# Performance work log

Hardware: AMD Instinct MI355X
Metric: run time of the kernel (lower is better)

Reference implementation:

```python
import jax, jax.numpy as jnp
import numpy as np

B, N, C1, C2, H = 4, 4096, 320, 256, 5
HD = C1 // H  # 64


def setup_inputs() -> dict:
    key = jax.random.key(0)
    ks = jax.random.split(key, 9)
    w = lambda k, shape, fan_in: jax.random.normal(k, shape, jnp.float32) * (fan_in ** -0.5)
    return {
        "x1": jax.random.normal(ks[0], (B, N, C1), jnp.float32),
        "x2": jax.random.normal(ks[1], (B, N, C2), jnp.float32),
        # nn.Linear weights, torch layout [out_features, in_features]
        "q1_w": w(ks[2], (C1, C1), C1),
        "q2_w": w(ks[3], (C1, C2), C2),
        "kv1_w": w(ks[4], (2 * C1, C2), C2),
        "kv2_w": w(ks[5], (2 * C1, C1), C1),
        "proj1_w": w(ks[6], (C1, C1), C1),
        "proj1_b": jnp.zeros((C1,), jnp.float32),
        "proj2_w": w(ks[7], (C1, C1), C1),
        "proj2_b": jnp.zeros((C1,), jnp.float32),
    }


def _branch(xq, xkv, q_w, kv_w, proj_w, proj_b):
    b, n, _ = xq.shape
    scale = HD ** -0.5
    q = (xq @ q_w.T).reshape(b, n, H, HD).transpose(0, 2, 1, 3)          # [B,H,N,HD]
    kv = (xkv @ kv_w.T).reshape(b, n, 2, H, HD).transpose(2, 0, 3, 1, 4)  # [2,B,H,N,HD]
    k, v = kv[0], kv[1]
    attn = jax.nn.softmax(jnp.einsum('bhqd,bhkd->bhqk', q * scale, k), axis=-1)
    y = jnp.einsum('bhqk,bhkd->bhqd', attn, v)                            # [B,H,N,HD]
    y = y.transpose(0, 2, 1, 3).reshape(b, n, C1)
    return y @ proj_w.T + proj_b


def reference(x1, x2, q1_w, q2_w, kv1_w, kv2_w, proj1_w, proj1_b, proj2_w, proj2_b):
    y1 = _branch(x1, x2, q1_w, kv1_w, proj1_w, proj1_b)  # x1 queries, x2 keys/values
    y2 = _branch(x2, x1, q2_w, kv2_w, proj2_w, proj2_b)  # x2 queries, x1 keys/values
    return jnp.concatenate((y1, y2), axis=-1)            # [B,N,2*C1]
```

## Files before the change

### kernel.cpp

```cpp
#include <hip/hip_runtime.h>
#include <hip/hip_bf16.h>

#define Bb 4
#define Nn 4096
#define C1 320
#define C2 256
#define Hh 5
#define HD 64
#define Mm (Bb*Nn)

using bf16 = __hip_bfloat16;
typedef __attribute__((ext_vector_type(8))) short  short8;
typedef __attribute__((ext_vector_type(4))) short  short4_;
typedef __attribute__((ext_vector_type(4))) float  f32x4;
typedef __attribute__((ext_vector_type(16))) float f32x16;

__device__ __forceinline__ short f2s(float f) {
    bf16 h = __float2bfloat16(f);
    short s;
    __builtin_memcpy(&s, &h, 2);
    return s;
}

__device__ __forceinline__ float fexp2(float x) {
#if __has_builtin(__builtin_amdgcn_exp2f)
    return __builtin_amdgcn_exp2f(x);
#else
    return exp2f(x);
#endif
}

__device__ __forceinline__ int swz(int row, int bb) {
    return row * 64 + ((bb ^ (row & 7)) << 3);
}

__device__ __forceinline__ unsigned cvtpk(float lo, float hi) {
    unsigned r;
    asm("v_cvt_pk_bf16_f32 %0, %1, %2" : "=v"(r) : "v"(lo), "v"(hi));
    return r;
}

__device__ __forceinline__ void plswap(unsigned &a, unsigned &b) {
#if __has_builtin(__builtin_amdgcn_permlane32_swap)
    auto r = __builtin_amdgcn_permlane32_swap(a, b, false, false);
    a = r[0]; b = r[1];
#else
    asm("v_permlane32_swap_b32 %0, %1" : "+v"(a), "+v"(b));
#endif
}

__device__ __forceinline__ short8 mk8(unsigned d0, unsigned d1, unsigned d2, unsigned d3) {
    union { unsigned u[4]; short8 s; } u;
    u.u[0] = d0; u.u[1] = d1; u.u[2] = d2; u.u[3] = d3;
    return u.s;
}

struct CvtArgs {
    const float* s[8];
    bf16* d[8];
    int off[9];
};

__global__ void cvt_all(CvtArgs a) {
    int i = (blockIdx.x * blockDim.x + threadIdx.x) * 4;
    if (i >= a.off[8]) return;
    int seg = 0;
    #pragma unroll
    for (int k = 1; k < 8; ++k) seg += (i >= a.off[k]);
    int j = i - a.off[seg];
    float4 v = *(const float4*)(a.s[seg] + j);
    short4_ o = { f2s(v.x), f2s(v.y), f2s(v.z), f2s(v.w) };
    *(short4_*)(a.d[seg] + j) = o;
}

__global__ __launch_bounds__(256) void gemm_bt(
    const bf16* __restrict__ A, const bf16* __restrict__ W,
    int K, int mode, float oscale,
    bf16* __restrict__ O1, bf16* __restrict__ O2,
    const float* __restrict__ bias, float* __restrict__ Of, int ooff)
{
    __shared__ bf16 la[64 * 64];
    __shared__ bf16 lw[64 * 64];
    const int m0 = blockIdx.x * 64, n0 = blockIdx.y * 64;
    const int t = threadIdx.x;
    const int wave = t >> 6, lane = t & 63, l16 = lane & 15, quad = lane >> 4;
    const int sr = t >> 3, sb = t & 7;

    f32x4 acc[4] = {{0.f,0.f,0.f,0.f},{0.f,0.f,0.f,0.f},{0.f,0.f,0.f,0.f},{0.f,0.f,0.f,0.f}};

    const int nk = K >> 6;
    short8 ra0 = *(const short8*)(A + (size_t)(m0 + sr) * K + sb * 8);
    short8 ra1 = *(const short8*)(A + (size_t)(m0 + sr + 32) * K + sb * 8);
    short8 rw0 = *(const short8*)(W + (size_t)(n0 + sr) * K + sb * 8);
    short8 rw1 = *(const short8*)(W + (size_t)(n0 + sr + 32) * K + sb * 8);

    for (int kt = 0; kt < nk; ++kt) {
        __syncthreads();
        *(short8*)&la[swz(sr, sb)]      = ra0;
        *(short8*)&la[swz(sr + 32, sb)] = ra1;
        *(short8*)&lw[swz(sr, sb)]      = rw0;
        *(short8*)&lw[swz(sr + 32, sb)] = rw1;
        __syncthreads();
        if (kt + 1 < nk) {
            const int k0 = (kt + 1) * 64;
            ra0 = *(const short8*)(A + (size_t)(m0 + sr) * K + k0 + sb * 8);
            ra1 = *(const short8*)(A + (size_t)(m0 + sr + 32) * K + k0 + sb * 8);
            rw0 = *(const short8*)(W + (size_t)(n0 + sr) * K + k0 + sb * 8);
            rw1 = *(const short8*)(W + (size_t)(n0 + sr + 32) * K + k0 + sb * 8);
        }
        const int arow = wave * 16 + l16;
        short8 a0 = *(const short8*)&la[swz(arow, quad)];
        short8 a1 = *(const short8*)&la[swz(arow, quad + 4)];
        #pragma unroll
        for (int nt = 0; nt < 4; ++nt) {
            const int brow = nt * 16 + l16;
            short8 b0 = *(const short8*)&lw[swz(brow, quad)];
            short8 b1 = *(const short8*)&lw[swz(brow, quad + 4)];
            acc[nt] = __builtin_amdgcn_mfma_f32_16x16x32_bf16(a0, b0, acc[nt], 0, 0, 0);
            acc[nt] = __builtin_amdgcn_mfma_f32_16x16x32_bf16(a1, b1, acc[nt], 0, 0, 0);
        }
    }

    const int mrow = m0 + wave * 16 + quad * 4;
    if (mode == 2) {
        #pragma unroll
        for (int nt = 0; nt < 4; ++nt) {
            int col = n0 + nt * 16 + l16;
            float bv = bias[col];
            #pragma unroll
            for (int r = 0; r < 4; ++r)
                Of[(size_t)(mrow + r) * 640 + ooff + col] = acc[nt][r] + bv;
        }
    } else if (mode == 0 || n0 < C1) {
        #pragma unroll
        for (int nt = 0; nt < 4; ++nt) {
            int col = n0 + nt * 16 + l16;
            #pragma unroll
            for (int r = 0; r < 4; ++r)
                O1[(size_t)(mrow + r) * C1 + col] = __float2bfloat16(acc[nt][r] * oscale);
        }
    } else {
        #pragma unroll
        for (int nt = 0; nt < 4; ++nt) {
            int col = n0 + nt * 16 + l16 - C1;
            int h = col >> 6, d = col & 63;
            #pragma unroll
            for (int r = 0; r < 4; ++r) {
                int m = mrow + r;
                int b = m >> 12, n = m & (Nn - 1);
                O2[((size_t)(b * Hh + h) * 64 + d) * Nn + n] = __float2bfloat16(acc[nt][r]);
            }
        }
    }
}

__global__ __launch_bounds__(256, 2) void flash_kernel(
    const bf16* __restrict__ Q1, const bf16* __restrict__ K1,
    const bf16* __restrict__ V1, bf16* __restrict__ Y1,
    const bf16* __restrict__ Q2, const bf16* __restrict__ K2,
    const bf16* __restrict__ V2, bf16* __restrict__ Y2)
{
    __shared__ bf16 lk[64 * 64];
    __shared__ bf16 lv[64 * 64];
    const int qt = blockIdx.x, h = blockIdx.y, z = blockIdx.z;
    const int b = z & 3, branch = z >> 2;
    const bf16* Q  = branch ? Q2 : Q1;
    const bf16* Km = branch ? K2 : K1;
    const bf16* Vt = branch ? V2 : V1;
    bf16*       Yo = branch ? Y2 : Y1;

    const int t = threadIdx.x;
    const int wave = t >> 6, lane = t & 63;
    const int l32 = lane & 31, hi = lane >> 5;
    const int sr = t >> 3, sb = t & 7;

    const int qrow0 = qt * 256 + wave * 64;

    short8 qf[2][4];
    #pragma unroll
    for (int qb = 0; qb < 2; ++qb) {
        const bf16* qptr = Q + (size_t)(b * Nn + qrow0 + qb * 32 + l32) * C1 + h * HD + hi * 8;
        #pragma unroll
        for (int ksd = 0; ksd < 4; ++ksd)
            qf[qb][ksd] = *(const short8*)(qptr + ksd * 16);
    }

    f32x16 o[2][2];
    #pragma unroll
    for (int qb = 0; qb < 2; ++qb)
        #pragma unroll
        for (int db = 0; db < 2; ++db)
            o[qb][db] = (f32x16){0.f,0.f,0.f,0.f,0.f,0.f,0.f,0.f,0.f,0.f,0.f,0.f,0.f,0.f,0.f,0.f};
    float lsum[2] = {0.f, 0.f};

    const bf16* Kbase = Km + (size_t)b * Nn * C1 + h * HD;
    const bf16* Vbase = Vt + (size_t)(b * Hh + h) * 64 * Nn;

    short8 rk0 = *(const short8*)(Kbase + (size_t)sr * C1 + sb * 8);
    short8 rk1 = *(const short8*)(Kbase + (size_t)(sr + 32) * C1 + sb * 8);
    short8 rv0 = *(const short8*)(Vbase + (size_t)sr * Nn + sb * 8);
    short8 rv1 = *(const short8*)(Vbase + (size_t)(sr + 32) * Nn + sb * 8);

    const int NT = Nn / 64;
    for (int kt = 0; kt < NT; ++kt) {
        __syncthreads();
        *(short8*)&lk[swz(sr, sb)]      = rk0;
        *(short8*)&lk[swz(sr + 32, sb)] = rk1;
        *(short8*)&lv[swz(sr, sb)]      = rv0;
        *(short8*)&lv[swz(sr + 32, sb)] = rv1;
        __syncthreads();
        if (kt + 1 < NT) {
            const int kn = (kt + 1) * 64;
            rk0 = *(const short8*)(Kbase + (size_t)(kn + sr) * C1 + sb * 8);
            rk1 = *(const short8*)(Kbase + (size_t)(kn + sr + 32) * C1 + sb * 8);
            rv0 = *(const short8*)(Vbase + (size_t)sr * Nn + kn + sb * 8);
            rv1 = *(const short8*)(Vbase + (size_t)(sr + 32) * Nn + kn + sb * 8);
        }

        #pragma unroll
        for (int kb = 0; kb < 2; ++kb) {
            short8 ka[4];
            #pragma unroll
            for (int ksd = 0; ksd < 4; ++ksd)
                ka[ksd] = *(const short8*)&lk[swz(kb * 32 + l32, ksd * 2 + hi)];

            short8 pa[2][2];
            #pragma unroll
            for (int qb = 0; qb < 2; ++qb) {
                f32x16 s = (f32x16){0.f,0.f,0.f,0.f,0.f,0.f,0.f,0.f,0.f,0.f,0.f,0.f,0.f,0.f,0.f,0.f};
                #pragma unroll
                for (int ksd = 0; ksd < 4; ++ksd)
                    s = __builtin_amdgcn_mfma_f32_32x32x16_bf16(ka[ksd], qf[qb][ksd], s, 0, 0, 0);
                float p[16];
                #pragma unroll
                for (int r = 0; r < 16; ++r) p[r] = fexp2(s[r]);
                lsum[qb] += (((p[0]+p[1])+(p[2]+p[3])) + ((p[4]+p[5])+(p[6]+p[7])))
                          + (((p[8]+p[9])+(p[10]+p[11])) + ((p[12]+p[13])+(p[14]+p[15])));
                unsigned d0 = cvtpk(p[0],  p[1]),  d2 = cvtpk(p[4],  p[5]);
                plswap(d0, d2);
                unsigned d1 = cvtpk(p[2],  p[3]),  d3 = cvtpk(p[6],  p[7]);
                plswap(d1, d3);
                pa[qb][0] = mk8(d0, d1, d2, d3);
                unsigned e0 = cvtpk(p[8],  p[9]),  e2 = cvtpk(p[12], p[13]);
                plswap(e0, e2);
                unsigned e1 = cvtpk(p[10], p[11]), e3 = cvtpk(p[14], p[15]);
                plswap(e1, e3);
                pa[qb][1] = mk8(e0, e1, e2, e3);
            }

            #pragma unroll
            for (int ks = 0; ks < 2; ++ks) {
                #pragma unroll
                for (int db = 0; db < 2; ++db) {
                    short8 bv = *(const short8*)&lv[swz(db * 32 + l32, kb * 4 + ks * 2 + hi)];
                    o[0][db] = __builtin_amdgcn_mfma_f32_32x32x16_bf16(pa[0][ks], bv, o[0][db], 0, 0, 0);
                    o[1][db] = __builtin_amdgcn_mfma_f32_32x32x16_bf16(pa[1][ks], bv, o[1][db], 0, 0, 0);
                }
            }
        }
    }

    #pragma unroll
    for (int qb = 0; qb < 2; ++qb) {
        float l = lsum[qb] + __shfl_xor(lsum[qb], 32, 64);
        float inv = 1.0f / l;
        #pragma unroll
        for (int r = 0; r < 16; ++r) {
            const int qr = (r & 3) + 8 * (r >> 2) + 4 * hi;
            float invr = __shfl(inv, qr, 64);
            size_t row = (size_t)(b * Nn + qrow0 + qb * 32 + qr);
            #pragma unroll
            for (int db = 0; db < 2; ++db)
                Yo[row * C1 + h * HD + db * 32 + l32] = __float2bfloat16(o[qb][db][r] * invr);
        }
    }
}

extern "C" void kernel_launch(void* const* d_in, const int* in_sizes, int n_in,
                              void* d_out, int out_size, void* d_ws, size_t ws_size,
                              hipStream_t stream)
{
    const float* x1   = (const float*)d_in[0];
    const float* x2   = (const float*)d_in[1];
    const float* q1w  = (const float*)d_in[2];
    const float* q2w  = (const float*)d_in[3];
    const float* kv1w = (const float*)d_in[4];
    const float* kv2w = (const float*)d_in[5];
    const float* p1w  = (const float*)d_in[6];
    const float* p1b  = (const float*)d_in[7];
    const float* p2w  = (const float*)d_in[8];
    const float* p2b  = (const float*)d_in[9];
    float* out = (float*)d_out;

    bf16* ws = (bf16*)d_ws;
    size_t o = 0;
    bf16* x1b  = ws + o; o += (size_t)Mm * C1;
    bf16* x2b  = ws + o; o += (size_t)Mm * C2;
    bf16* wq1  = ws + o; o += C1 * C1;
    bf16* wq2  = ws + o; o += C1 * C2;
    bf16* wkv1 = ws + o; o += 2 * C1 * C2;
    bf16* wkv2 = ws + o; o += 2 * C1 * C1;
    bf16* wp1  = ws + o; o += C1 * C1;
    bf16* wp2  = ws + o; o += C1 * C1;
    bf16* Q1   = ws + o; o += (size_t)Mm * C1;
    bf16* K1   = ws + o; o += (size_t)Mm * C1;
    bf16* V1t  = ws + o; o += (size_t)Mm * C1;
    bf16* Q2   = ws + o; o += (size_t)Mm * C1;
    bf16* K2   = ws + o; o += (size_t)Mm * C1;
    bf16* V2t  = ws + o; o += (size_t)Mm * C1;
    bf16* Y1   = ws + o; o += (size_t)Mm * C1;
    bf16* Y2   = ws + o; o += (size_t)Mm * C1;
    (void)ws_size; (void)in_sizes; (void)n_in; (void)out_size;

    CvtArgs ca;
    ca.s[0] = x1;   ca.d[0] = x1b;  int n0 = Mm * C1;
    ca.s[1] = x2;   ca.d[1] = x2b;  int n1 = Mm * C2;
    ca.s[2] = q1w;  ca.d[2] = wq1;  int n2 = C1 * C1;
    ca.s[3] = q2w;  ca.d[3] = wq2;  int n3 = C1 * C2;
    ca.s[4] = kv1w; ca.d[4] = wkv1; int n4 = 2 * C1 * C2;
    ca.s[5] = kv2w; ca.d[5] = wkv2; int n5 = 2 * C1 * C1;
    ca.s[6] = p1w;  ca.d[6] = wp1;  int n6 = C1 * C1;
    ca.s[7] = p2w;  ca.d[7] = wp2;  int n7 = C1 * C1;
    int ns[8] = {n0, n1, n2, n3, n4, n5, n6, n7};
    ca.off[0] = 0;
    for (int i = 0; i < 8; ++i) ca.off[i + 1] = ca.off[i] + ns[i];
    int total = ca.off[8];
    cvt_all<<<dim3((total / 4 + 255) / 256), 256, 0, stream>>>(ca);

    const float QS = 0.125f * 1.4426950408889634f;

    gemm_bt<<<dim3(Mm / 64, C1 / 64), 256, 0, stream>>>(x1b, wq1, C1, 0, QS, Q1, nullptr, nullptr, nullptr, 0);
    gemm_bt<<<dim3(Mm / 64, (2 * C1) / 64), 256, 0, stream>>>(x2b, wkv1, C2, 1, 1.0f, K1, V1t, nullptr, nullptr, 0);
    gemm_bt<<<dim3(Mm / 64, C1 / 64), 256, 0, stream>>>(x2b, wq2, C2, 0, QS, Q2, nullptr, nullptr, nullptr, 0);
    gemm_bt<<<dim3(Mm / 64, (2 * C1) / 64), 256, 0, stream>>>(x1b, wkv2, C1, 1, 1.0f, K2, V2t, nullptr, nullptr, 0);

    flash_kernel<<<dim3(Nn / 256, Hh, 2 * Bb), 256, 0, stream>>>(Q1, K1, V1t, Y1, Q2, K2, V2t, Y2);

    gemm_bt<<<dim3(Mm / 64, C1 / 64), 256, 0, stream>>>(Y1, wp1, C1, 2, 1.0f, nullptr, nullptr, p1b, out, 0);
    gemm_bt<<<dim3(Mm / 64, C1 / 64), 256, 0, stream>>>(Y2, wp2, C1, 2, 1.0f, nullptr, nullptr, p2b, out, C1);
}
```

Measured before the change: 351.6 us.

## Double-buffer K/V tiles in LDS, compute row sums via MFMA, add setprio

The flash kernel now keeps two LDS buffers for K and V. The next tile is written into the other buffer while the current one is being computed, which cuts the loop to one barrier per iteration and lets loads run two tiles ahead. The softmax denominator now comes from extra MFMAs against a ones vector instead of scalar adds and cross-lane shuffles. It also uses bf16-rounded probabilities, which slightly changes numerics. s_setprio hints are placed around the MFMA groups. The cost is double the LDS use, which may affect occupancy at 2 blocks/CU, plus four more MFMAs per kb step.

```diff
diff --git a/kernel.cpp b/kernel.cpp
--- a/kernel.cpp
+++ b/kernel.cpp
@@ -160,8 +160,8 @@
     const bf16* __restrict__ Q2, const bf16* __restrict__ K2,
     const bf16* __restrict__ V2, bf16* __restrict__ Y2)
 {
-    __shared__ bf16 lk[64 * 64];
-    __shared__ bf16 lv[64 * 64];
+    __shared__ bf16 lk[2][64 * 64];
+    __shared__ bf16 lv[2][64 * 64];
     const int qt = blockIdx.x, h = blockIdx.y, z = blockIdx.z;
     const int b = z & 3, branch = z >> 2;
     const bf16* Q  = branch ? Q2 : Q1;
@@ -185,36 +185,63 @@
             qf[qb][ksd] = *(const short8*)(qptr + ksd * 16);
     }
 
+    const f32x16 Z = {0.f,0.f,0.f,0.f,0.f,0.f,0.f,0.f,0.f,0.f,0.f,0.f,0.f,0.f,0.f,0.f};
+    const short  one_bf = (short)0x3F80;
+    const short8 ONESB = {one_bf,one_bf,one_bf,one_bf,one_bf,one_bf,one_bf,one_bf};
+
     f32x16 o[2][2];
+    f32x16 lacc[2];
     #pragma unroll
-    for (int qb = 0; qb < 2; ++qb)
-        #pragma unroll
-        for (int db = 0; db < 2; ++db)
-            o[qb][db] = (f32x16){0.f,0.f,0.f,0.f,0.f,0.f,0.f,0.f,0.f,0.f,0.f,0.f,0.f,0.f,0.f,0.f};
-    float lsum[2] = {0.f, 0.f};
+    for (int qb = 0; qb < 2; ++qb) {
+        lacc[qb] = Z;
+        #pragma unroll
+        for (int db = 0; db < 2; ++db) o[qb][db] = Z;
+    }
 
     const bf16* Kbase = Km + (size_t)b * Nn * C1 + h * HD;
     const bf16* Vbase = Vt + (size_t)(b * Hh + h) * 64 * Nn;
 
-    short8 rk0 = *(const short8*)(Kbase + (size_t)sr * C1 + sb * 8);
-    short8 rk1 = *(const short8*)(Kbase + (size_t)(sr + 32) * C1 + sb * 8);
-    short8 rv0 = *(const short8*)(Vbase + (size_t)sr * Nn + sb * 8);
-    short8 rv1 = *(const short8*)(Vbase + (size_t)(sr + 32) * Nn + sb * 8);
+    const bf16* kp0 = Kbase + (size_t)sr * C1 + sb * 8;
+    const bf16* kp1 = kp0 + (size_t)32 * C1;
+    const bf16* vp0 = Vbase + (size_t)sr * Nn + sb * 8;
+    const bf16* vp1 = vp0 + (size_t)32 * Nn;
+
+    short8 rk0 = *(const short8*)kp0;
+    short8 rk1 = *(const short8*)kp1;
+    short8 rv0 = *(const short8*)vp0;
+    short8 rv1 = *(const short8*)vp1;
+    kp0 += 64 * C1; kp1 += 64 * C1; vp0 += 64; vp1 += 64;
+    *(short8*)&lk[0][swz(sr, sb)]      = rk0;
+    *(short8*)&lk[0][swz(sr + 32, sb)] = rk1;
+    *(short8*)&lv[0][swz(sr, sb)]      = rv0;
+    *(short8*)&lv[0][swz(sr + 32, sb)] = rv1;
+    rk0 = *(const short8*)kp0;
+    rk1 = *(const short8*)kp1;
+    rv0 = *(const short8*)vp0;
+    rv1 = *(const short8*)vp1;
+    kp0 += 64 * C1; kp1 += 64 * C1; vp0 += 64; vp1 += 64;
+    __syncthreads();
 
     const int NT = Nn / 64;
     for (int kt = 0; kt < NT; ++kt) {
-        __syncthreads();
-        *(short8*)&lk[swz(sr, sb)]      = rk0;
-        *(short8*)&lk[swz(sr + 32, sb)] = rk1;
-        *(short8*)&lv[swz(sr, sb)]      = rv0;
-        *(short8*)&lv[swz(sr + 32, sb)] = rv1;
-        __syncthreads();
+        const int cur = kt & 1;
+        const bf16* LK = lk[cur];
+        const bf16* LV = lv[cur];
+
         if (kt + 1 < NT) {
-            const int kn = (kt + 1) * 64;
-            rk0 = *(const short8*)(Kbase + (size_t)(kn + sr) * C1 + sb * 8);
-            rk1 = *(const short8*)(Kbase + (size_t)(kn + sr + 32) * C1 + sb * 8);
-            rv0 = *(const short8*)(Vbase + (size_t)sr * Nn + kn + sb * 8);
-            rv1 = *(const short8*)(Vbase + (size_t)(sr + 32) * Nn + kn + sb * 8);
+            bf16* WK = lk[cur ^ 1];
+            bf16* WV = lv[cur ^ 1];
+            *(short8*)&WK[swz(sr, sb)]      = rk0;
+            *(short8*)&WK[swz(sr + 32, sb)] = rk1;
+            *(short8*)&WV[swz(sr, sb)]      = rv0;
+            *(short8*)&WV[swz(sr + 32, sb)] = rv1;
+        }
+        if (kt + 2 < NT) {
+            rk0 = *(const short8*)kp0;
+            rk1 = *(const short8*)kp1;
+            rv0 = *(const short8*)vp0;
+            rv1 = *(const short8*)vp1;
+            kp0 += 64 * C1; kp1 += 64 * C1; vp0 += 64; vp1 += 64;
         }
 
         #pragma unroll
@@ -222,20 +249,20 @@
             short8 ka[4];
             #pragma unroll
             for (int ksd = 0; ksd < 4; ++ksd)
-                ka[ksd] = *(const short8*)&lk[swz(kb * 32 + l32, ksd * 2 + hi)];
+                ka[ksd] = *(const short8*)&LK[swz(kb * 32 + l32, ksd * 2 + hi)];
 
             short8 pa[2][2];
             #pragma unroll
             for (int qb = 0; qb < 2; ++qb) {
-                f32x16 s = (f32x16){0.f,0.f,0.f,0.f,0.f,0.f,0.f,0.f,0.f,0.f,0.f,0.f,0.f,0.f,0.f,0.f};
-                #pragma unroll
-                for (int ksd = 0; ksd < 4; ++ksd)
-                    s = __builtin_amdgcn_mfma_f32_32x32x16_bf16(ka[ksd], qf[qb][ksd], s, 0, 0, 0);
+                __builtin_amdgcn_s_setprio(1);
+                f32x16 s = __builtin_amdgcn_mfma_f32_32x32x16_bf16(ka[0], qf[qb][0], Z, 0, 0, 0);
+                s = __builtin_amdgcn_mfma_f32_32x32x16_bf16(ka[1], qf[qb][1], s, 0, 0, 0);
+                s = __builtin_amdgcn_mfma_f32_32x32x16_bf16(ka[2], qf[qb][2], s, 0, 0, 0);
+                s = __builtin_amdgcn_mfma_f32_32x32x16_bf16(ka[3], qf[qb][3], s, 0, 0, 0);
+                __builtin_amdgcn_s_setprio(0);
                 float p[16];
                 #pragma unroll
                 for (int r = 0; r < 16; ++r) p[r] = fexp2(s[r]);
-                lsum[qb] += (((p[0]+p[1])+(p[2]+p[3])) + ((p[4]+p[5])+(p[6]+p[7])))
-                          + (((p[8]+p[9])+(p[10]+p[11])) + ((p[12]+p[13])+(p[14]+p[15])));
                 unsigned d0 = cvtpk(p[0],  p[1]),  d2 = cvtpk(p[4],  p[5]);
                 plswap(d0, d2);
                 unsigned d1 = cvtpk(p[2],  p[3]),  d3 = cvtpk(p[6],  p[7]);
@@ -248,26 +275,29 @@
                 pa[qb][1] = mk8(e0, e1, e2, e3);
             }
 
+            __builtin_amdgcn_s_setprio(1);
             #pragma unroll
             for (int ks = 0; ks < 2; ++ks) {
                 #pragma unroll
                 for (int db = 0; db < 2; ++db) {
-                    short8 bv = *(const short8*)&lv[swz(db * 32 + l32, kb * 4 + ks * 2 + hi)];
+                    short8 bv = *(const short8*)&LV[swz(db * 32 + l32, kb * 4 + ks * 2 + hi)];
                     o[0][db] = __builtin_amdgcn_mfma_f32_32x32x16_bf16(pa[0][ks], bv, o[0][db], 0, 0, 0);
                     o[1][db] = __builtin_amdgcn_mfma_f32_32x32x16_bf16(pa[1][ks], bv, o[1][db], 0, 0, 0);
                 }
+                lacc[0] = __builtin_amdgcn_mfma_f32_32x32x16_bf16(pa[0][ks], ONESB, lacc[0], 0, 0, 0);
+                lacc[1] = __builtin_amdgcn_mfma_f32_32x32x16_bf16(pa[1][ks], ONESB, lacc[1], 0, 0, 0);
             }
-        }
+            __builtin_amdgcn_s_setprio(0);
+        }
+        __syncthreads();
     }
 
     #pragma unroll
     for (int qb = 0; qb < 2; ++qb) {
-        float l = lsum[qb] + __shfl_xor(lsum[qb], 32, 64);
-        float inv = 1.0f / l;
         #pragma unroll
         for (int r = 0; r < 16; ++r) {
             const int qr = (r & 3) + 8 * (r >> 2) + 4 * hi;
-            float invr = __shfl(inv, qr, 64);
+            float invr = 1.0f / lacc[qb][r];
             size_t row = (size_t)(b * Nn + qrow0 + qb * 32 + qr);
             #pragma unroll
             for (int db = 0; db < 2; ++db)
```

Result: slower. 366.5 us (+4.2%).

## Split flash attention key range across two wave groups with LDS reduction

Applied to the files above, without the earlier changes.

Doubles the flash kernel block to 512 threads, with waves 0-3 and waves 4-7 each processing half of the key sequence (0-2047 vs 2048-4095) for the same 256 query rows. Each group loads its own 32-key tile per iteration, and at the end the partial row sums and output accumulators are combined through shared memory before the first group normalizes and writes. This is meant to raise the number of waves in flight and cover latency, since the grid only has 640 blocks. In exchange it adds a final reduction with several barriers and more register pressure under the new 512,4 launch bound.

```diff
diff --git a/kernel.cpp b/kernel.cpp
--- a/kernel.cpp
+++ b/kernel.cpp
@@ -154,7 +154,7 @@
     }
 }
 
-__global__ __launch_bounds__(256, 2) void flash_kernel(
+__global__ __launch_bounds__(512, 4) void flash_kernel(
     const bf16* __restrict__ Q1, const bf16* __restrict__ K1,
     const bf16* __restrict__ V1, bf16* __restrict__ Y1,
     const bf16* __restrict__ Q2, const bf16* __restrict__ K2,
@@ -172,9 +172,10 @@
     const int t = threadIdx.x;
     const int wave = t >> 6, lane = t & 63;
     const int l32 = lane & 31, hi = lane >> 5;
+    const int qw = wave & 3, khalf = wave >> 2;
     const int sr = t >> 3, sb = t & 7;
 
-    const int qrow0 = qt * 256 + wave * 64;
+    const int qrow0 = qt * 256 + qw * 64;
 
     short8 qf[2][4];
     #pragma unroll
@@ -196,82 +197,109 @@
     const bf16* Kbase = Km + (size_t)b * Nn * C1 + h * HD;
     const bf16* Vbase = Vt + (size_t)(b * Hh + h) * 64 * Nn;
 
-    short8 rk0 = *(const short8*)(Kbase + (size_t)sr * C1 + sb * 8);
-    short8 rk1 = *(const short8*)(Kbase + (size_t)(sr + 32) * C1 + sb * 8);
-    short8 rv0 = *(const short8*)(Vbase + (size_t)sr * Nn + sb * 8);
-    short8 rv1 = *(const short8*)(Vbase + (size_t)(sr + 32) * Nn + sb * 8);
-
-    const int NT = Nn / 64;
+    const bf16* kp = Kbase + (size_t)((sr >> 5) * 2048 + (sr & 31)) * C1 + sb * 8;
+    const bf16* vp = Vbase + (size_t)sr * Nn + (sb >> 2) * 2048 + (sb & 3) * 8;
+    short8 rk = *(const short8*)kp;
+    short8 rv = *(const short8*)vp;
+
+    const int NT = 2048 / 32;
     for (int kt = 0; kt < NT; ++kt) {
         __syncthreads();
-        *(short8*)&lk[swz(sr, sb)]      = rk0;
-        *(short8*)&lk[swz(sr + 32, sb)] = rk1;
-        *(short8*)&lv[swz(sr, sb)]      = rv0;
-        *(short8*)&lv[swz(sr + 32, sb)] = rv1;
+        *(short8*)&lk[swz(sr, sb)] = rk;
+        *(short8*)&lv[swz(sr, sb)] = rv;
         __syncthreads();
         if (kt + 1 < NT) {
-            const int kn = (kt + 1) * 64;
-            rk0 = *(const short8*)(Kbase + (size_t)(kn + sr) * C1 + sb * 8);
-            rk1 = *(const short8*)(Kbase + (size_t)(kn + sr + 32) * C1 + sb * 8);
-            rv0 = *(const short8*)(Vbase + (size_t)sr * Nn + kn + sb * 8);
-            rv1 = *(const short8*)(Vbase + (size_t)(sr + 32) * Nn + kn + sb * 8);
-        }
-
-        #pragma unroll
-        for (int kb = 0; kb < 2; ++kb) {
-            short8 ka[4];
+            kp += 32 * C1; vp += 32;
+            rk = *(const short8*)kp;
+            rv = *(const short8*)vp;
+        }
+
+        short8 ka[4];
+        #pragma unroll
+        for (int ksd = 0; ksd < 4; ++ksd)
+            ka[ksd] = *(const short8*)&lk[swz(khalf * 32 + l32, ksd * 2 + hi)];
+
+        short8 pa[2][2];
+        #pragma unroll
+        for (int qb = 0; qb < 2; ++qb) {
+            f32x16 s = (f32x16){0.f,0.f,0.f,0.f,0.f,0.f,0.f,0.f,0.f,0.f,0.f,0.f,0.f,0.f,0.f,0.f};
             #pragma unroll
             for (int ksd = 0; ksd < 4; ++ksd)
-                ka[ksd] = *(const short8*)&lk[swz(kb * 32 + l32, ksd * 2 + hi)];
-
-            short8 pa[2][2];
-            #pragma unroll
-            for (int qb = 0; qb < 2; ++qb) {
-                f32x16 s = (f32x16){0.f,0.f,0.f,0.f,0.f,0.f,0.f,0.f,0.f,0.f,0.f,0.f,0.f,0.f,0.f,0.f};
-                #pragma unroll
-                for (int ksd = 0; ksd < 4; ++ksd)
-                    s = __builtin_amdgcn_mfma_f32_32x32x16_bf16(ka[ksd], qf[qb][ksd], s, 0, 0, 0);
-                float p[16];
-                #pragma unroll
-                for (int r = 0; r < 16; ++r) p[r] = fexp2(s[r]);
-                lsum[qb] += (((p[0]+p[1])+(p[2]+p[3])) + ((p[4]+p[5])+(p[6]+p[7])))
-                          + (((p[8]+p[9])+(p[10]+p[11])) + ((p[12]+p[13])+(p[14]+p[15])));
-                unsigned d0 = cvtpk(p[0],  p[1]),  d2 = cvtpk(p[4],  p[5]);
-                plswap(d0, d2);
-                unsigned d1 = cvtpk(p[2],  p[3]),  d3 = cvtpk(p[6],  p[7]);
-                plswap(d1, d3);
-                pa[qb][0] = mk8(d0, d1, d2, d3);
-                unsigned e0 = cvtpk(p[8],  p[9]),  e2 = cvtpk(p[12], p[13]);
-                plswap(e0, e2);
-                unsigned e1 = cvtpk(p[10], p[11]), e3 = cvtpk(p[14], p[15]);
-                plswap(e1, e3);
-                pa[qb][1] = mk8(e0, e1, e2, e3);
-            }
-
-            #pragma unroll
-            for (int ks = 0; ks < 2; ++ks) {
-                #pragma unroll
-                for (int db = 0; db < 2; ++db) {
-                    short8 bv = *(const short8*)&lv[swz(db * 32 + l32, kb * 4 + ks * 2 + hi)];
-                    o[0][db] = __builtin_amdgcn_mfma_f32_32x32x16_bf16(pa[0][ks], bv, o[0][db], 0, 0, 0);
-                    o[1][db] = __builtin_amdgcn_mfma_f32_32x32x16_bf16(pa[1][ks], bv, o[1][db], 0, 0, 0);
-                }
-            }
-        }
-    }
+                s = __builtin_amdgcn_mfma_f32_32x32x16_bf16(ka[ksd], qf[qb][ksd], s, 0, 0, 0);
+            float p[16];
+            #pragma unroll
+            for (int r = 0; r < 16; ++r) p[r] = fexp2(s[r]);
+            lsum[qb] += (((p[0]+p[1])+(p[2]+p[3])) + ((p[4]+p[5])+(p[6]+p[7])))
+                      + (((p[8]+p[9])+(p[10]+p[11])) + ((p[12]+p[13])+(p[14]+p[15])));
+            unsigned d0 = cvtpk(p[0],  p[1]),  d2 = cvtpk(p[4],  p[5]);
+            plswap(d0, d2);
+            unsigned d1 = cvtpk(p[2],  p[3]),  d3 = cvtpk(p[6],  p[7]);
+            plswap(d1, d3);
+            pa[qb][0] = mk8(d0, d1, d2, d3);
+            unsigned e0 = cvtpk(p[8],  p[9]),  e2 = cvtpk(p[12], p[13]);
+            plswap(e0, e2);
+            unsigned e1 = cvtpk(p[10], p[11]), e3 = cvtpk(p[14], p[15]);
+            plswap(e1, e3);
+            pa[qb][1] = mk8(e0, e1, e2, e3);
+        }
+
+        #pragma unroll
+        for (int ks = 0; ks < 2; ++ks) {
+            #pragma unroll
+            for (int db = 0; db < 2; ++db) {
+                short8 bv = *(const short8*)&lv[swz(db * 32 + l32, khalf * 4 + ks * 2 + hi)];
+                o[0][db] = __builtin_amdgcn_mfma_f32_32x32x16_bf16(pa[0][ks], bv, o[0][db], 0, 0, 0);
+                o[1][db] = __builtin_amdgcn_mfma_f32_32x32x16_bf16(pa[1][ks], bv, o[1][db], 0, 0, 0);
+            }
+        }
+    }
+
+    __syncthreads();
+    float* sk = (float*)lk;
+    float* sv = (float*)lv;
+    const int idx = qw * 64 + lane;
+
+    if (khalf == 1) { sk[idx] = lsum[0]; sk[256 + idx] = lsum[1]; }
+    __syncthreads();
+    if (khalf == 0) { lsum[0] += sk[idx]; lsum[1] += sk[256 + idx]; }
 
     #pragma unroll
     for (int qb = 0; qb < 2; ++qb) {
-        float l = lsum[qb] + __shfl_xor(lsum[qb], 32, 64);
-        float inv = 1.0f / l;
-        #pragma unroll
-        for (int r = 0; r < 16; ++r) {
-            const int qr = (r & 3) + 8 * (r >> 2) + 4 * hi;
-            float invr = __shfl(inv, qr, 64);
-            size_t row = (size_t)(b * Nn + qrow0 + qb * 32 + qr);
-            #pragma unroll
-            for (int db = 0; db < 2; ++db)
-                Yo[row * C1 + h * HD + db * 32 + l32] = __float2bfloat16(o[qb][db][r] * invr);
+        #pragma unroll
+        for (int db = 0; db < 2; ++db) {
+            __syncthreads();
+            if (khalf == 1) {
+                #pragma unroll
+                for (int r = 0; r < 16; ++r) {
+                    float* dst = (r < 8) ? sk : sv;
+                    dst[(r & 7) * 256 + idx] = o[qb][db][r];
+                }
+            }
+            __syncthreads();
+            if (khalf == 0) {
+                #pragma unroll
+                for (int r = 0; r < 16; ++r) {
+                    const float* src = (r < 8) ? sk : sv;
+                    o[qb][db][r] += src[(r & 7) * 256 + idx];
+                }
+            }
+        }
+    }
+
+    if (khalf == 0) {
+        #pragma unroll
+        for (int qb = 0; qb < 2; ++qb) {
+            float l = lsum[qb] + __shfl_xor(lsum[qb], 32, 64);
+            float inv = 1.0f / l;
+            #pragma unroll
+            for (int r = 0; r < 16; ++r) {
+                const int qr = (r & 3) + 8 * (r >> 2) + 4 * hi;
+                float invr = __shfl(inv, qr, 64);
+                size_t row = (size_t)(b * Nn + qrow0 + qb * 32 + qr);
+                #pragma unroll
+                for (int db = 0; db < 2; ++db)
+                    Yo[row * C1 + h * HD + db * 32 + l32] = __float2bfloat16(o[qb][db][r] * invr);
+            }
         }
     }
 }
@@ -334,7 +362,7 @@
     gemm_bt<<<dim3(Mm / 64, C1 / 64), 256, 0, stream>>>(x2b, wq2, C2, 0, QS, Q2, nullptr, nullptr, nullptr, 0);
     gemm_bt<<<dim3(Mm / 64, (2 * C1) / 64), 256, 0, stream>>>(x1b, wkv2, C1, 1, 1.0f, K2, V2t, nullptr, nullptr, 0);
 
-    flash_kernel<<<dim3(Nn / 256, Hh, 2 * Bb), 256, 0, stream>>>(Q1, K1, V1t, Y1, Q2, K2, V2t, Y2);
+    flash_kernel<<<dim3(Nn / 256, Hh, 2 * Bb), 512, 0, stream>>>(Q1, K1, V1t, Y1, Q2, K2, V2t, Y2);
 
     gemm_bt<<<dim3(Mm / 64, C1 / 64), 256, 0, stream>>>(Y1, wp1, C1, 2, 1.0f, nullptr, nullptr, p1b, out, 0);
     gemm_bt<<<dim3(Mm / 64, C1 / 64), 256, 0, stream>>>(Y2, wp2, C1, 2, 1.0f, nullptr, nullptr, p2b, out, C1);
```

New measurement: 796.9 us. 127% more time.

## Merge projection GEMMs per input and enlarge GEMM tiles to 128 rows

Applied to the files above, without the earlier changes.

The four Q/KV projection GEMMs become two launches, one per input activation. Each launch computes both the Q and the KV outputs for that input, so the input is shared across one grid. The two output-projection GEMMs become a single launch with a z dimension. The M tile grows from 64 to 128 rows, so each wave computes two 16-row fragments and reuses the B fragments from shared memory. This cuts launch count and the number of times weights are reloaded, at the cost of more registers and LDS per block and fewer blocks.

```diff
diff --git a/kernel.cpp b/kernel.cpp
--- a/kernel.cpp
+++ b/kernel.cpp
@@ -13,7 +13,6 @@
 typedef __attribute__((ext_vector_type(8))) short  short8;
 typedef __attribute__((ext_vector_type(4))) short  short4_;
 typedef __attribute__((ext_vector_type(4))) float  f32x4;
-typedef __attribute__((ext_vector_type(16))) float f32x16;
 
 __device__ __forceinline__ short f2s(float f) {
     bf16 h = __float2bfloat16(f);
@@ -32,6 +31,209 @@
 
 __device__ __forceinline__ int swz(int row, int bb) {
     return row * 64 + ((bb ^ (row & 7)) << 3);
+}
+
+struct CvtArgs {
+    const float* s[8];
+    bf16* d[8];
+    int off[9];
+};
+
+__global__ void cvt_all(CvtArgs a) {
+    int i = (blockIdx.x * blockDim.x + threadIdx.x) * 4;
+    if (i >= a.off[8]) return;
+    int seg = 0;
+    #pragma unroll
+    for (int k = 1; k < 8; ++k) seg += (i >= a.off[k]);
+    int j = i - a.off[seg];
+    float4 v = *(const float4*)(a.s[seg] + j);
+    short4_ o = { f2s(v.x), f2s(v.y), f2s(v.z), f2s(v.w) };
+    *(short4_*)(a.d[seg] + j) = o;
+}
+
+__global__ __launch_bounds__(256) void gemm_proj(
+    const bf16* __restrict__ A, const bf16* __restrict__ Wq,
+    const bf16* __restrict__ Wkv, int K, float qs,
+    bf16* __restrict__ Qo, bf16* __restrict__ Ko, bf16* __restrict__ Vo)
+{
+    __shared__ bf16 la[128 * 64];
+    __shared__ bf16 lw[64 * 64];
+    const int m0 = blockIdx.x * 128;
+    const bool isq = blockIdx.y < 5;
+    const bf16* W = isq ? Wq : Wkv;
+    const int n0 = (isq ? blockIdx.y : blockIdx.y - 5) * 64;
+    const int t = threadIdx.x;
+    const int wave = t >> 6, lane = t & 63, l16 = lane & 15, quad = lane >> 4;
+    const int sr = t >> 3, sb = t & 7;
+
+    f32x4 acc[2][4];
+    #pragma unroll
+    for (int mf = 0; mf < 2; ++mf)
+        #pragma unroll
+        for (int nt = 0; nt < 4; ++nt) acc[mf][nt] = {0.f,0.f,0.f,0.f};
+
+    const int nk = K >> 6;
+    const bf16* ap = A + (size_t)(m0 + sr) * K + sb * 8;
+    const bf16* wp = W + (size_t)(n0 + sr) * K + sb * 8;
+    short8 ra0 = *(const short8*)ap;
+    short8 ra1 = *(const short8*)(ap + (size_t)32 * K);
+    short8 ra2 = *(const short8*)(ap + (size_t)64 * K);
+    short8 ra3 = *(const short8*)(ap + (size_t)96 * K);
+    short8 rw0 = *(const short8*)wp;
+    short8 rw1 = *(const short8*)(wp + (size_t)32 * K);
+
+    for (int kt = 0; kt < nk; ++kt) {
+        __syncthreads();
+        *(short8*)&la[swz(sr,      sb)] = ra0;
+        *(short8*)&la[swz(sr + 32, sb)] = ra1;
+        *(short8*)&la[swz(sr + 64, sb)] = ra2;
+        *(short8*)&la[swz(sr + 96, sb)] = ra3;
+        *(short8*)&lw[swz(sr,      sb)] = rw0;
+        *(short8*)&lw[swz(sr + 32, sb)] = rw1;
+        __syncthreads();
+        if (kt + 1 < nk) {
+            ap += 64; wp += 64;
+            ra0 = *(const short8*)ap;
+            ra1 = *(const short8*)(ap + (size_t)32 * K);
+            ra2 = *(const short8*)(ap + (size_t)64 * K);
+            ra3 = *(const short8*)(ap + (size_t)96 * K);
+            rw0 = *(const short8*)wp;
+            rw1 = *(const short8*)(wp + (size_t)32 * K);
+        }
+        const int arow = wave * 32 + l16;
+        short8 a00 = *(const short8*)&la[swz(arow,      quad)];
+        short8 a01 = *(const short8*)&la[swz(arow,      quad + 4)];
+        short8 a10 = *(const short8*)&la[swz(arow + 16, quad)];
+        short8 a11 = *(const short8*)&la[swz(arow + 16, quad + 4)];
+        #pragma unroll
+        for (int nt = 0; nt < 4; ++nt) {
+            const int brow = nt * 16 + l16;
+            short8 b0 = *(const short8*)&lw[swz(brow, quad)];
+            short8 b1 = *(const short8*)&lw[swz(brow, quad + 4)];
+            acc[0][nt] = __builtin_amdgcn_mfma_f32_16x16x32_bf16(a00, b0, acc[0][nt], 0, 0, 0);
+            acc[0][nt] = __builtin_amdgcn_mfma_f32_16x16x32_bf16(a01, b1, acc[0][nt], 0, 0, 0);
+            acc[1][nt] = __builtin_amdgcn_mfma_f32_16x16x32_bf16(a10, b0, acc[1][nt], 0, 0, 0);
+            acc[1][nt] = __builtin_amdgcn_mfma_f32_16x16x32_bf16(a11, b1, acc[1][nt], 0, 0, 0);
+        }
+    }
+
+    const bool isv = !isq && n0 >= C1;
+    #pragma unroll
+    for (int mf = 0; mf < 2; ++mf) {
+        const int mrow = m0 + wave * 32 + mf * 16 + quad * 4;
+        if (isq) {
+            #pragma unroll
+            for (int nt = 0; nt < 4; ++nt) {
+                int col = n0 + nt * 16 + l16;
+                #pragma unroll
+                for (int r = 0; r < 4; ++r)
+                    Qo[(size_t)(mrow + r) * C1 + col] = __float2bfloat16(acc[mf][nt][r] * qs);
+            }
+        } else if (!isv) {
+            #pragma unroll
+            for (int nt = 0; nt < 4; ++nt) {
+                int col = n0 + nt * 16 + l16;
+                #pragma unroll
+                for (int r = 0; r < 4; ++r)
+                    Ko[(size_t)(mrow + r) * C1 + col] = __float2bfloat16(acc[mf][nt][r]);
+            }
+        } else {
+            #pragma unroll
+            for (int nt = 0; nt < 4; ++nt) {
+                int col = n0 + nt * 16 + l16 - C1;
+                int h = col >> 6, d = col & 63;
+                #pragma unroll
+                for (int r = 0; r < 4; ++r) {
+                    int m = mrow + r;
+                    int b = m >> 12, n = m & (Nn - 1);
+                    Vo[((size_t)(b * Hh + h) * 64 + d) * Nn + n] = __float2bfloat16(acc[mf][nt][r]);
+                }
+            }
+        }
+    }
+}
+
+__global__ __launch_bounds__(256) void gemm_out(
+    const bf16* __restrict__ Y1, const bf16* __restrict__ Wp1, const float* __restrict__ B1,
+    const bf16* __restrict__ Y2, const bf16* __restrict__ Wp2, const float* __restrict__ B2,
+    float* __restrict__ Of)
+{
+    __shared__ bf16 la[128 * 64];
+    __shared__ bf16 lw[64 * 64];
+    const int zz = blockIdx.z;
+    const bf16* A = zz ? Y2 : Y1;
+    const bf16* W = zz ? Wp2 : Wp1;
+    const float* bias = zz ? B2 : B1;
+    const int ooff = zz ? C1 : 0;
+    const int m0 = blockIdx.x * 128, n0 = blockIdx.y * 64;
+    const int t = threadIdx.x;
+    const int wave = t >> 6, lane = t & 63, l16 = lane & 15, quad = lane >> 4;
+    const int sr = t >> 3, sb = t & 7;
+    const int K = C1;
+
+    f32x4 acc[2][4];
+    #pragma unroll
+    for (int mf = 0; mf < 2; ++mf)
+        #pragma unroll
+        for (int nt = 0; nt < 4; ++nt) acc[mf][nt] = {0.f,0.f,0.f,0.f};
+
+    const int nk = K >> 6;
+    const bf16* ap = A + (size_t)(m0 + sr) * K + sb * 8;
+    const bf16* wp = W + (size_t)(n0 + sr) * K + sb * 8;
+    short8 ra0 = *(const short8*)ap;
+    short8 ra1 = *(const short8*)(ap + (size_t)32 * K);
+    short8 ra2 = *(const short8*)(ap + (size_t)64 * K);
+    short8 ra3 = *(const short8*)(ap + (size_t)96 * K);
+    short8 rw0 = *(const short8*)wp;
+    short8 rw1 = *(const short8*)(wp + (size_t)32 * K);
+
+    for (int kt = 0; kt < nk; ++kt) {
+        __syncthreads();
+        *(short8*)&la[swz(sr,      sb)] = ra0;
+        *(short8*)&la[swz(sr + 32, sb)] = ra1;
+        *(short8*)&la[swz(sr + 64, sb)] = ra2;
+        *(short8*)&la[swz(sr + 96, sb)] = ra3;
+        *(short8*)&lw[swz(sr,      sb)] = rw0;
+        *(short8*)&lw[swz(sr + 32, sb)] = rw1;
+        __syncthreads();
+        if (kt + 1 < nk) {
+            ap += 64; wp += 64;
+            ra0 = *(const short8*)ap;
+            ra1 = *(const short8*)(ap + (size_t)32 * K);
+            ra2 = *(const short8*)(ap + (size_t)64 * K);
+            ra3 = *(const short8*)(ap + (size_t)96 * K);
+            rw0 = *(const short8*)wp;
+            rw1 = *(const short8*)(wp + (size_t)32 * K);
+        }
+        const int arow = wave * 32 + l16;
+        short8 a00 = *(const short8*)&la[swz(arow,      quad)];
+        short8 a01 = *(const short8*)&la[swz(arow,      quad + 4)];
+        short8 a10 = *(const short8*)&la[swz(arow + 16, quad)];
+        short8 a11 = *(const short8*)&la[swz(arow + 16, quad + 4)];
+        #pragma unroll
+        for (int nt = 0; nt < 4; ++nt) {
+            const int brow = nt * 16 + l16;
+            short8 b0 = *(const short8*)&lw[swz(brow, quad)];
+            short8 b1 = *(const short8*)&lw[swz(brow, quad + 4)];
+            acc[0][nt] = __builtin_amdgcn_mfma_f32_16x16x32_bf16(a00, b0, acc[0][nt], 0, 0, 0);
+            acc[0][nt] = __builtin_amdgcn_mfma_f32_16x16x32_bf16(a01, b1, acc[0][nt], 0, 0, 0);
+            acc[1][nt] = __builtin_amdgcn_mfma_f32_16x16x32_bf16(a10, b0, acc[1][nt], 0, 0, 0);
+            acc[1][nt] = __builtin_amdgcn_mfma_f32_16x16x32_bf16(a11, b1, acc[1][nt], 0, 0, 0);
+        }
+    }
+
+    #pragma unroll
+    for (int mf = 0; mf < 2; ++mf) {
+        const int mrow = m0 + wave * 32 + mf * 16 + quad * 4;
+        #pragma unroll
+        for (int nt = 0; nt < 4; ++nt) {
+            int col = n0 + nt * 16 + l16;
+            float bv = bias[col];
+            #pragma unroll
+            for (int r = 0; r < 4; ++r)
+                Of[(size_t)(mrow + r) * 640 + ooff + col] = acc[mf][nt][r] + bv;
+        }
+    }
 }
 
 __device__ __forceinline__ unsigned cvtpk(float lo, float hi) {
@@ -55,104 +257,7 @@
     return u.s;
 }
 
-struct CvtArgs {
-    const float* s[8];
-    bf16* d[8];
-    int off[9];
-};
-
-__global__ void cvt_all(CvtArgs a) {
-    int i = (blockIdx.x * blockDim.x + threadIdx.x) * 4;
-    if (i >= a.off[8]) return;
-    int seg = 0;
-    #pragma unroll
-    for (int k = 1; k < 8; ++k) seg += (i >= a.off[k]);
-    int j = i - a.off[seg];
-    float4 v = *(const float4*)(a.s[seg] + j);
-    short4_ o = { f2s(v.x), f2s(v.y), f2s(v.z), f2s(v.w) };
-    *(short4_*)(a.d[seg] + j) = o;
-}
-
-__global__ __launch_bounds__(256) void gemm_bt(
-    const bf16* __restrict__ A, const bf16* __restrict__ W,
-    int K, int mode, float oscale,
-    bf16* __restrict__ O1, bf16* __restrict__ O2,
-    const float* __restrict__ bias, float* __restrict__ Of, int ooff)
-{
-    __shared__ bf16 la[64 * 64];
-    __shared__ bf16 lw[64 * 64];
-    const int m0 = blockIdx.x * 64, n0 = blockIdx.y * 64;
-    const int t = threadIdx.x;
-    const int wave = t >> 6, lane = t & 63, l16 = lane & 15, quad = lane >> 4;
-    const int sr = t >> 3, sb = t & 7;
-
-    f32x4 acc[4] = {{0.f,0.f,0.f,0.f},{0.f,0.f,0.f,0.f},{0.f,0.f,0.f,0.f},{0.f,0.f,0.f,0.f}};
-
-    const int nk = K >> 6;
-    short8 ra0 = *(const short8*)(A + (size_t)(m0 + sr) * K + sb * 8);
-    short8 ra1 = *(const short8*)(A + (size_t)(m0 + sr + 32) * K + sb * 8);
-    short8 rw0 = *(const short8*)(W + (size_t)(n0 + sr) * K + sb * 8);
-    short8 rw1 = *(const short8*)(W + (size_t)(n0 + sr + 32) * K + sb * 8);
-
-    for (int kt = 0; kt < nk; ++kt) {
-        __syncthreads();
-        *(short8*)&la[swz(sr, sb)]      = ra0;
-        *(short8*)&la[swz(sr + 32, sb)] = ra1;
-        *(short8*)&lw[swz(sr, sb)]      = rw0;
-        *(short8*)&lw[swz(sr + 32, sb)] = rw1;
-        __syncthreads();
-        if (kt + 1 < nk) {
-            const int k0 = (kt + 1) * 64;
-            ra0 = *(const short8*)(A + (size_t)(m0 + sr) * K + k0 + sb * 8);
-            ra1 = *(const short8*)(A + (size_t)(m0 + sr + 32) * K + k0 + sb * 8);
-            rw0 = *(const short8*)(W + (size_t)(n0 + sr) * K + k0 + sb * 8);
-            rw1 = *(const short8*)(W + (size_t)(n0 + sr + 32) * K + k0 + sb * 8);
-        }
-        const int arow = wave * 16 + l16;
-        short8 a0 = *(const short8*)&la[swz(arow, quad)];
-        short8 a1 = *(const short8*)&la[swz(arow, quad + 4)];
-        #pragma unroll
-        for (int nt = 0; nt < 4; ++nt) {
-            const int brow = nt * 16 + l16;
-            short8 b0 = *(const short8*)&lw[swz(brow, quad)];
-            short8 b1 = *(const short8*)&lw[swz(brow, quad + 4)];
-            acc[nt] = __builtin_amdgcn_mfma_f32_16x16x32_bf16(a0, b0, acc[nt], 0, 0, 0);
-            acc[nt] = __builtin_amdgcn_mfma_f32_16x16x32_bf16(a1, b1, acc[nt], 0, 0, 0);
-        }
-    }
-
-    const int mrow = m0 + wave * 16 + quad * 4;
-    if (mode == 2) {
-        #pragma unroll
-        for (int nt = 0; nt < 4; ++nt) {
-            int col = n0 + nt * 16 + l16;
-            float bv = bias[col];
-            #pragma unroll
-            for (int r = 0; r < 4; ++r)
-                Of[(size_t)(mrow + r) * 640 + ooff + col] = acc[nt][r] + bv;
-        }
-    } else if (mode == 0 || n0 < C1) {
-        #pragma unroll
-        for (int nt = 0; nt < 4; ++nt) {
-            int col = n0 + nt * 16 + l16;
-            #pragma unroll
-            for (int r = 0; r < 4; ++r)
-                O1[(size_t)(mrow + r) * C1 + col] = __float2bfloat16(acc[nt][r] * oscale);
-        }
-    } else {
-        #pragma unroll
-        for (int nt = 0; nt < 4; ++nt) {
-            int col = n0 + nt * 16 + l16 - C1;
-            int h = col >> 6, d = col & 63;
-            #pragma unroll
-            for (int r = 0; r < 4; ++r) {
-                int m = mrow + r;
-                int b = m >> 12, n = m & (Nn - 1);
-                O2[((size_t)(b * Hh + h) * 64 + d) * Nn + n] = __float2bfloat16(acc[nt][r]);
-            }
-        }
-    }
-}
+typedef __attribute__((ext_vector_type(16))) float f32x16;
 
 __global__ __launch_bounds__(256, 2) void flash_kernel(
     const bf16* __restrict__ Q1, const bf16* __restrict__ K1,
@@ -329,13 +434,10 @@
 
     const float QS = 0.125f * 1.4426950408889634f;
 
-    gemm_bt<<<dim3(Mm / 64, C1 / 64), 256, 0, stream>>>(x1b, wq1, C1, 0, QS, Q1, nullptr, nullptr, nullptr, 0);
-    gemm_bt<<<dim3(Mm / 64, (2 * C1) / 64), 256, 0, stream>>>(x2b, wkv1, C2, 1, 1.0f, K1, V1t, nullptr, nullptr, 0);
-    gemm_bt<<<dim3(Mm / 64, C1 / 64), 256, 0, stream>>>(x2b, wq2, C2, 0, QS, Q2, nullptr, nullptr, nullptr, 0);
-    gemm_bt<<<dim3(Mm / 64, (2 * C1) / 64), 256, 0, stream>>>(x1b, wkv2, C1, 1, 1.0f, K2, V2t, nullptr, nullptr, 0);
+    gemm_proj<<<dim3(Mm / 128, 15), 256, 0, stream>>>(x1b, wq1, wkv2, C1, QS, Q1, K2, V2t);
+    gemm_proj<<<dim3(Mm / 128, 15), 256, 0, stream>>>(x2b, wq2, wkv1, C2, QS, Q2, K1, V1t);
 
     flash_kernel<<<dim3(Nn / 256, Hh, 2 * Bb), 256, 0, stream>>>(Q1, K1, V1t, Y1, Q2, K2, V2t, Y2);
 
-    gemm_bt<<<dim3(Mm / 64, C1 / 64), 256, 0, stream>>>(Y1, wp1, C1, 2, 1.0f, nullptr, nullptr, p1b, out, 0);
-    gemm_bt<<<dim3(Mm / 64, C1 / 64), 256, 0, stream>>>(Y2, wp2, C1, 2, 1.0f, nullptr, nullptr, p2b, out, C1);
-}
+    gemm_out<<<dim3(Mm / 128, C1 / 64, 2), 256, 0, stream>>>(Y1, wp1, p1b, Y2, wp2, p2b, out);
+}
```

Result: no change. 351.0 us (-0.2%).
